# Kernel optimization log

Hardware: AMD Instinct MI355X
Metric: run time of the kernel (lower is better)

The kernel has to match this reference:

```python
import jax, jax.numpy as jnp
import numpy as np

B, C = 65536, 1000
EPS = float(np.finfo(np.float32).eps)

def setup_inputs() -> dict:
    key = jax.random.key(0)
    k1, k2, k3 = jax.random.split(key, 3)
    return {
        "Simple_vector": jax.random.normal(k1, (B, C), dtype=jnp.float32),
        "label_list": jax.random.randint(k2, (B,), 0, C),
        "w_L": jax.random.normal(k3, (C,), dtype=jnp.float32),
        "w_H": jnp.ones((1,), dtype=jnp.float32),
        "b": jnp.ones((1,), dtype=jnp.float32),
    }

def reference(Simple_vector, label_list, w_L, w_H, b):
    C_ = Simple_vector.shape[1]
    # LTS: per-row dot with class-weight vector
    LTS = Simple_vector @ w_L  # (B,)
    # H_hat = sum_i p_i * log p_i  (negative entropy), single stable pass
    logp = jax.nn.log_softmax(Simple_vector, axis=1)
    H_hat = jnp.sum(jnp.exp(logp) * logp, axis=1)  # (B,)
    HTS = w_H[0] * (H_hat / jnp.log(jnp.float32(C_))) + b[0]
    a = LTS + HTS
    T = jnp.clip(jax.nn.softplus(a), EPS, None)  # (B,)
    scaled = Simple_vector / T[:, None]
    # mean cross-entropy
    ls = jax.nn.log_softmax(scaled, axis=1)
    nll = -jnp.take_along_axis(ls, label_list[:, None], axis=1)[:, 0]
    return jnp.mean(nll)
```

## Files before the change

kernel.cpp:

```cpp
#include <hip/hip_runtime.h>
#include <float.h>
#include <math.h>


static constexpr int   kC4    = 250;
static constexpr int   kBlock = 256;
static constexpr int   kGrid  = 2048;
static constexpr int   kWavesTotal = kGrid * (kBlock / 64);
static constexpr int   kRPW   = 8;
static constexpr float kEps   = 1.1920928955078125e-07f;
static constexpr float kLogC  = 6.907755279f;

__device__ __forceinline__ float wred_max(float v) {
#pragma unroll
  for (int off = 32; off > 0; off >>= 1) v = fmaxf(v, __shfl_xor(v, off, 64));
  return v;
}
__device__ __forceinline__ float wred_sum(float v) {
#pragma unroll
  for (int off = 32; off > 0; off >>= 1) v += __shfl_xor(v, off, 64);
  return v;
}

__device__ __forceinline__ void p1_dot_max(const float4 c, const float4 w,
                                           float& L, float& m) {
  L = fmaf(c.x, w.x, L); L = fmaf(c.y, w.y, L);
  L = fmaf(c.z, w.z, L); L = fmaf(c.w, w.w, L);
  m = fmaxf(m, fmaxf(fmaxf(c.x, c.y), fmaxf(c.z, c.w)));
}
__device__ __forceinline__ void p2_sumexp(const float4 c, const float m,
                                          float& S, float& W) {
  float e;
  e = __expf(c.x - m); S += e; W = fmaf(e, c.x, W);
  e = __expf(c.y - m); S += e; W = fmaf(e, c.y, W);
  e = __expf(c.z - m); S += e; W = fmaf(e, c.z, W);
  e = __expf(c.w - m); S += e; W = fmaf(e, c.w, W);
}
__device__ __forceinline__ void p3_sumexp2(const float4 c, const float rT,
                                           const float nmrT, float& S2) {
  S2 += __expf(fmaf(c.x, rT, nmrT)); S2 += __expf(fmaf(c.y, rT, nmrT));
  S2 += __expf(fmaf(c.z, rT, nmrT)); S2 += __expf(fmaf(c.w, rT, nmrT));
}
__device__ __forceinline__ float pick_lab(const float4 v, const int el) {
  return (el == 0) ? v.x : (el == 1) ? v.y : (el == 2) ? v.z : v.w;
}

#define SENT4 make_float4(-FLT_MAX, -FLT_MAX, -FLT_MAX, -FLT_MAX)

__device__ __forceinline__ float row_nll(
    const float4 c0, const float4 c1, const float4 c2, const float4 c3,
    const float4 w0, const float4 w1, const float4 w2, const float4 w3,
    const int labc, const float wH0, const float b0) {
  float L = 0.f, m = -FLT_MAX;
  p1_dot_max(c0, w0, L, m); p1_dot_max(c1, w1, L, m);
  p1_dot_max(c2, w2, L, m); p1_dot_max(c3, w3, L, m);
  m = wred_max(m);

  float S = 0.f, W = 0.f;
  p2_sumexp(c0, m, S, W); p2_sumexp(c1, m, S, W);
  p2_sumexp(c2, m, S, W); p2_sumexp(c3, m, S, W);
  S = wred_sum(S);
  W = wred_sum(W);
  L = wred_sum(L);

  const int c4l = labc >> 2;
  const int sl  = c4l >> 6, ln = c4l & 63, el = labc & 3;
  float4 v = (sl == 0) ? c0 : (sl == 1) ? c1 : (sl == 2) ? c2 : c3;
  const float xl = __shfl(pick_lab(v, el), ln, 64);

  const float Hhat = W / S - m - __logf(S);
  const float a    = L + wH0 * (Hhat / kLogC) + b0;
  const float sp   = (a > 0.f) ? (a + log1pf(__expf(-a))) : log1pf(__expf(a));
  const float T    = fmaxf(sp, kEps);
  const float rT   = 1.0f / T;
  const float nmrT = -m * rT;

  float S2 = 0.f;
  p3_sumexp2(c0, rT, nmrT, S2); p3_sumexp2(c1, rT, nmrT, S2);
  p3_sumexp2(c2, rT, nmrT, S2); p3_sumexp2(c3, rT, nmrT, S2);
  S2 = wred_sum(S2);

  return __logf(S2) - fmaf(xl, rT, nmrT);
}

__global__ __launch_bounds__(kBlock, 4) void ats_row_kernel_d2(
    const float* __restrict__ X, const int* __restrict__ labels,
    const float* __restrict__ wL, const float* __restrict__ wH,
    const float* __restrict__ bb, double* __restrict__ partial) {
  const int lane   = threadIdx.x & 63;
  const int wib    = threadIdx.x >> 6;
  const int wid    = blockIdx.x * (kBlock / 64) + wib;
  const bool tailok = lane < (kC4 - 192);

  const float4* WLr = reinterpret_cast<const float4*>(wL);
  const float4 w0 = WLr[lane];
  const float4 w1 = WLr[64 + lane];
  const float4 w2 = WLr[128 + lane];
  const float4 w3 = tailok ? WLr[192 + lane] : make_float4(0.f, 0.f, 0.f, 0.f);
  const float wH0 = wH[0];
  const float b0  = bb[0];

  double acc = 0.0;
  const int base = wid * kRPW;

  float4 a0, a1, a2, a3, b0_, b1_, b2_, b3_;
  int labA, labB;
  {
    const float4* Xa = reinterpret_cast<const float4*>(X) + (size_t)base * kC4;
    a0 = Xa[lane]; a1 = Xa[64 + lane]; a2 = Xa[128 + lane];
    a3 = tailok ? Xa[192 + lane] : SENT4;
    labA = labels[base];
    const float4* Xb = Xa + kC4;
    b0_ = Xb[lane]; b1_ = Xb[64 + lane]; b2_ = Xb[128 + lane];
    b3_ = tailok ? Xb[192 + lane] : SENT4;
    labB = labels[base + 1];
  }

#pragma unroll
  for (int i = 0; i < kRPW; ++i) {
    float4 n0 = SENT4, n1 = SENT4, n2 = SENT4, n3 = SENT4;
    int labN = 0;
    if (i + 2 < kRPW) {
      const float4* Xn =
          reinterpret_cast<const float4*>(X) + (size_t)(base + i + 2) * kC4;
      n0 = Xn[lane]; n1 = Xn[64 + lane]; n2 = Xn[128 + lane];
      n3 = tailok ? Xn[192 + lane] : SENT4;
      labN = labels[base + i + 2];
    }

    acc += (double)row_nll(a0, a1, a2, a3, w0, w1, w2, w3, labA, wH0, b0);

    a0 = b0_; a1 = b1_; a2 = b2_; a3 = b3_; labA = labB;
    b0_ = n0; b1_ = n1; b2_ = n2; b3_ = n3; labB = labN;
  }

  __shared__ double sacc[kBlock / 64];
  if (lane == 0) sacc[wib] = acc;
  __syncthreads();
  if (threadIdx.x == 0)
    partial[blockIdx.x] = (sacc[0] + sacc[1]) + (sacc[2] + sacc[3]);
}

__global__ __launch_bounds__(kBlock) void ats_row_kernel_gen(
    const float* __restrict__ X, const int* __restrict__ labels,
    const float* __restrict__ wL, const float* __restrict__ wH,
    const float* __restrict__ bb, double* __restrict__ partial, int B) {
  const int lane   = threadIdx.x & 63;
  const int wib    = threadIdx.x >> 6;
  const int wid    = blockIdx.x * (kBlock / 64) + wib;
  const bool tailok = lane < (kC4 - 192);

  const float4* WLr = reinterpret_cast<const float4*>(wL);
  const float4 w0 = WLr[lane];
  const float4 w1 = WLr[64 + lane];
  const float4 w2 = WLr[128 + lane];
  const float4 w3 = tailok ? WLr[192 + lane] : make_float4(0.f, 0.f, 0.f, 0.f);
  const float wH0 = wH[0];
  const float b0  = bb[0];

  double acc = 0.0;
  int row = wid;
  float4 c0, c1, c2, c3;
  int labc = 0;
  if (row < B) {
    const float4* Xr = reinterpret_cast<const float4*>(X) + (size_t)row * kC4;
    c0 = Xr[lane]; c1 = Xr[64 + lane]; c2 = Xr[128 + lane];
    c3 = tailok ? Xr[192 + lane] : SENT4;
    labc = labels[row];
  }
  for (; row < B; row += kWavesTotal) {
    const int nrow = row + kWavesTotal;
    float4 n0 = SENT4, n1 = SENT4, n2 = SENT4, n3 = SENT4;
    int labn = 0;
    if (nrow < B) {
      const float4* Xn = reinterpret_cast<const float4*>(X) + (size_t)nrow * kC4;
      n0 = Xn[lane]; n1 = Xn[64 + lane]; n2 = Xn[128 + lane];
      n3 = tailok ? Xn[192 + lane] : SENT4;
      labn = labels[nrow];
    }
    acc += (double)row_nll(c0, c1, c2, c3, w0, w1, w2, w3, labc, wH0, b0);
    c0 = n0; c1 = n1; c2 = n2; c3 = n3; labc = labn;
  }
  __shared__ double sacc[kBlock / 64];
  if (lane == 0) sacc[wib] = acc;
  __syncthreads();
  if (threadIdx.x == 0)
    partial[blockIdx.x] = (sacc[0] + sacc[1]) + (sacc[2] + sacc[3]);
}

__global__ __launch_bounds__(256) void ats_final_kernel(
    const double* __restrict__ partial, float* __restrict__ out, int n, int B) {
  __shared__ double sdata[256];
  double a = 0.0;
  for (int i = threadIdx.x; i < n; i += 256) a += partial[i];
  sdata[threadIdx.x] = a;
  __syncthreads();
#pragma unroll
  for (int s = 128; s > 0; s >>= 1) {
    if ((int)threadIdx.x < s) sdata[threadIdx.x] += sdata[threadIdx.x + s];
    __syncthreads();
  }
  if (threadIdx.x == 0) out[0] = (float)(sdata[0] / (double)B);
}

extern "C" void kernel_launch(void* const* d_in, const int* in_sizes, int n_in,
                              void* d_out, int out_size, void* d_ws, size_t ws_size,
                              hipStream_t stream) {
  (void)n_in; (void)out_size; (void)ws_size;
  const float* X   = (const float*)d_in[0];
  const int*   lab = (const int*)d_in[1];
  const float* wL  = (const float*)d_in[2];
  const float* wH  = (const float*)d_in[3];
  const float* bb  = (const float*)d_in[4];
  const int B = in_sizes[1];
  double* partial = (double*)d_ws;
  float* out = (float*)d_out;

  if (B == kWavesTotal * kRPW) {
    ats_row_kernel_d2<<<kGrid, kBlock, 0, stream>>>(X, lab, wL, wH, bb, partial);
  } else {
    ats_row_kernel_gen<<<kGrid, kBlock, 0, stream>>>(X, lab, wL, wH, bb,
                                                     partial, B);
  }
  ats_final_kernel<<<1, 256, 0, stream>>>(partial, out, kGrid, B);
}
```

Before: 62.30 us.

## Software-pipeline rows so pass three of one row overlaps the next row's reductions

```diff
diff --git a/kernel.cpp b/kernel.cpp
--- a/kernel.cpp
+++ b/kernel.cpp
@@ -21,6 +21,26 @@
   for (int off = 32; off > 0; off >>= 1) v += __shfl_xor(v, off, 64);
   return v;
 }
+__device__ __forceinline__ void wred_sum3(float& a, float& b, float& c) {
+#pragma unroll
+  for (int off = 32; off > 0; off >>= 1) {
+    const float ta = __shfl_xor(a, off, 64);
+    const float tb = __shfl_xor(b, off, 64);
+    const float tc = __shfl_xor(c, off, 64);
+    a += ta; b += tb; c += tc;
+  }
+}
+__device__ __forceinline__ void wred_sum4(float& a, float& b, float& c,
+                                          float& d) {
+#pragma unroll
+  for (int off = 32; off > 0; off >>= 1) {
+    const float ta = __shfl_xor(a, off, 64);
+    const float tb = __shfl_xor(b, off, 64);
+    const float tc = __shfl_xor(c, off, 64);
+    const float td = __shfl_xor(d, off, 64);
+    a += ta; b += tb; c += tc; d += td;
+  }
+}
 
 __device__ __forceinline__ void p1_dot_max(const float4 c, const float4 w,
                                            float& L, float& m) {
@@ -47,43 +67,7 @@
 
 #define SENT4 make_float4(-FLT_MAX, -FLT_MAX, -FLT_MAX, -FLT_MAX)
 
-__device__ __forceinline__ float row_nll(
-    const float4 c0, const float4 c1, const float4 c2, const float4 c3,
-    const float4 w0, const float4 w1, const float4 w2, const float4 w3,
-    const int labc, const float wH0, const float b0) {
-  float L = 0.f, m = -FLT_MAX;
-  p1_dot_max(c0, w0, L, m); p1_dot_max(c1, w1, L, m);
-  p1_dot_max(c2, w2, L, m); p1_dot_max(c3, w3, L, m);
-  m = wred_max(m);
-
-  float S = 0.f, W = 0.f;
-  p2_sumexp(c0, m, S, W); p2_sumexp(c1, m, S, W);
-  p2_sumexp(c2, m, S, W); p2_sumexp(c3, m, S, W);
-  S = wred_sum(S);
-  W = wred_sum(W);
-  L = wred_sum(L);
-
-  const int c4l = labc >> 2;
-  const int sl  = c4l >> 6, ln = c4l & 63, el = labc & 3;
-  float4 v = (sl == 0) ? c0 : (sl == 1) ? c1 : (sl == 2) ? c2 : c3;
-  const float xl = __shfl(pick_lab(v, el), ln, 64);
-
-  const float Hhat = W / S - m - __logf(S);
-  const float a    = L + wH0 * (Hhat / kLogC) + b0;
-  const float sp   = (a > 0.f) ? (a + log1pf(__expf(-a))) : log1pf(__expf(a));
-  const float T    = fmaxf(sp, kEps);
-  const float rT   = 1.0f / T;
-  const float nmrT = -m * rT;
-
-  float S2 = 0.f;
-  p3_sumexp2(c0, rT, nmrT, S2); p3_sumexp2(c1, rT, nmrT, S2);
-  p3_sumexp2(c2, rT, nmrT, S2); p3_sumexp2(c3, rT, nmrT, S2);
-  S2 = wred_sum(S2);
-
-  return __logf(S2) - fmaf(xl, rT, nmrT);
-}
-
-__global__ __launch_bounds__(kBlock, 4) void ats_row_kernel_d2(
+__global__ __launch_bounds__(kBlock, 4) void ats_row_kernel_df(
     const float* __restrict__ X, const int* __restrict__ labels,
     const float* __restrict__ wL, const float* __restrict__ wH,
     const float* __restrict__ bb, double* __restrict__ partial) {
@@ -116,6 +100,9 @@
     labB = labels[base + 1];
   }
 
+  float4 pa0, pa1, pa2, pa3;
+  float prT = 0.f, pnmrT = 0.f, pxl = 0.f;
+
 #pragma unroll
   for (int i = 0; i < kRPW; ++i) {
     float4 n0 = SENT4, n1 = SENT4, n2 = SENT4, n3 = SENT4;
@@ -128,10 +115,54 @@
       labN = labels[base + i + 2];
     }
 
-    acc += (double)row_nll(a0, a1, a2, a3, w0, w1, w2, w3, labA, wH0, b0);
+    float L = 0.f, mloc = -FLT_MAX;
+    p1_dot_max(a0, w0, L, mloc); p1_dot_max(a1, w1, L, mloc);
+    p1_dot_max(a2, w2, L, mloc); p1_dot_max(a3, w3, L, mloc);
+
+    float S2p = 0.f;
+    if (i > 0) {
+      p3_sumexp2(pa0, prT, pnmrT, S2p); p3_sumexp2(pa1, prT, pnmrT, S2p);
+      p3_sumexp2(pa2, prT, pnmrT, S2p); p3_sumexp2(pa3, prT, pnmrT, S2p);
+    }
+
+    const float m = wred_max(mloc);
+
+    const int c4l = labA >> 2;
+    const int sl  = c4l >> 6, ln = c4l & 63, el = labA & 3;
+    float4 v = (sl == 0) ? a0 : (sl == 1) ? a1 : (sl == 2) ? a2 : a3;
+    const float xl = __shfl(pick_lab(v, el), ln, 64);
+
+    float S = 0.f, W = 0.f;
+    p2_sumexp(a0, m, S, W); p2_sumexp(a1, m, S, W);
+    p2_sumexp(a2, m, S, W); p2_sumexp(a3, m, S, W);
+
+    if (i > 0) {
+      wred_sum4(S, W, L, S2p);
+      acc += (double)(__logf(S2p) - fmaf(pxl, prT, pnmrT));
+    } else {
+      wred_sum3(S, W, L);
+    }
+
+    const float Hhat = W / S - m - __logf(S);
+    const float aT   = L + wH0 * (Hhat / kLogC) + b0;
+    const float sp   = (aT > 0.f) ? (aT + log1pf(__expf(-aT)))
+                                  : log1pf(__expf(aT));
+    const float T    = fmaxf(sp, kEps);
+    const float rT   = 1.0f / T;
+
+    prT = rT; pnmrT = -m * rT; pxl = xl;
+    pa0 = a0; pa1 = a1; pa2 = a2; pa3 = a3;
 
     a0 = b0_; a1 = b1_; a2 = b2_; a3 = b3_; labA = labB;
     b0_ = n0; b1_ = n1; b2_ = n2; b3_ = n3; labB = labN;
+  }
+
+  {
+    float S2p = 0.f;
+    p3_sumexp2(pa0, prT, pnmrT, S2p); p3_sumexp2(pa1, prT, pnmrT, S2p);
+    p3_sumexp2(pa2, prT, pnmrT, S2p); p3_sumexp2(pa3, prT, pnmrT, S2p);
+    S2p = wred_sum(S2p);
+    acc += (double)(__logf(S2p) - fmaf(pxl, prT, pnmrT));
   }
 
   __shared__ double sacc[kBlock / 64];
@@ -139,6 +170,34 @@
   __syncthreads();
   if (threadIdx.x == 0)
     partial[blockIdx.x] = (sacc[0] + sacc[1]) + (sacc[2] + sacc[3]);
+}
+
+__device__ __forceinline__ float row_nll(
+    const float4 c0, const float4 c1, const float4 c2, const float4 c3,
+    const float4 w0, const float4 w1, const float4 w2, const float4 w3,
+    const int labc, const float wH0, const float b0) {
+  float L = 0.f, m = -FLT_MAX;
+  p1_dot_max(c0, w0, L, m); p1_dot_max(c1, w1, L, m);
+  p1_dot_max(c2, w2, L, m); p1_dot_max(c3, w3, L, m);
+  m = wred_max(m);
+  float S = 0.f, W = 0.f;
+  p2_sumexp(c0, m, S, W); p2_sumexp(c1, m, S, W);
+  p2_sumexp(c2, m, S, W); p2_sumexp(c3, m, S, W);
+  S = wred_sum(S); W = wred_sum(W); L = wred_sum(L);
+  const int c4l = labc >> 2;
+  const int sl = c4l >> 6, ln = c4l & 63, el = labc & 3;
+  float4 v = (sl == 0) ? c0 : (sl == 1) ? c1 : (sl == 2) ? c2 : c3;
+  const float xl = __shfl(pick_lab(v, el), ln, 64);
+  const float Hhat = W / S - m - __logf(S);
+  const float a = L + wH0 * (Hhat / kLogC) + b0;
+  const float sp = (a > 0.f) ? (a + log1pf(__expf(-a))) : log1pf(__expf(a));
+  const float T = fmaxf(sp, kEps);
+  const float rT = 1.0f / T, nmrT = -m * rT;
+  float S2 = 0.f;
+  p3_sumexp2(c0, rT, nmrT, S2); p3_sumexp2(c1, rT, nmrT, S2);
+  p3_sumexp2(c2, rT, nmrT, S2); p3_sumexp2(c3, rT, nmrT, S2);
+  S2 = wred_sum(S2);
+  return __logf(S2) - fmaf(xl, rT, nmrT);
 }
 
 __global__ __launch_bounds__(kBlock) void ats_row_kernel_gen(
@@ -217,7 +276,7 @@
   float* out = (float*)d_out;
 
   if (B == kWavesTotal * kRPW) {
-    ats_row_kernel_d2<<<kGrid, kBlock, 0, stream>>>(X, lab, wL, wH, bb, partial);
+    ats_row_kernel_df<<<kGrid, kBlock, 0, stream>>>(X, lab, wL, wH, bb, partial);
   } else {
     ats_row_kernel_gen<<<kGrid, kBlock, 0, stream>>>(X, lab, wL, wH, bb,
                                                      partial, B);
```

After: 62.14 us. No clear change (-0.3%).
